# Kernel tuning notes

Measured on AMD Instinct MI355X. Metric: run time of the kernel, lower is better.

## Reference

```python
import jax, jax.numpy as jnp
import numpy as np

B, T, C, HEAD = 4, 4096, 1024, 64
SCALE = 1.0 / (C ** 0.5)  # module divides by embedding_size**0.5, not head_size**0.5


def setup_inputs() -> dict:
    key = jax.random.key(0)
    kx, kq, kk, kv = jax.random.split(key, 4)
    x = jax.random.normal(kx, (B, T, C), dtype=jnp.float32)
    # nn.Linear(C, head_size, bias=False) weights, stored as (C, head_size) for x @ W
    Wq = jax.random.normal(kq, (C, HEAD), dtype=jnp.float32) * (1.0 / np.sqrt(C))
    Wk = jax.random.normal(kk, (C, HEAD), dtype=jnp.float32) * (1.0 / np.sqrt(C))
    Wv = jax.random.normal(kv, (C, HEAD), dtype=jnp.float32) * (1.0 / np.sqrt(C))
    return {"x": x, "Wq": Wq, "Wk": Wk, "Wv": Wv}


def reference(x, Wq, Wk, Wv):
    q = jnp.einsum('btc,ch->bth', x, Wq)  # [B,T,HEAD]
    k = jnp.einsum('btc,ch->bth', x, Wk)
    v = jnp.einsum('btc,ch->bth', x, Wv)
    aff = jnp.einsum('bqh,bkh->bqk', q, k) * SCALE  # [B,T,T]
    causal = jnp.tril(jnp.ones((T, T), dtype=bool))
    aff = jnp.where(causal, aff, -jnp.inf)
    p = jax.nn.softmax(aff, axis=-1)  # dropout p=0.0 -> identity
    return jnp.einsum('bqk,bkh->bqh', p, v)  # [B,T,HEAD]
```

## Files before the change

### kernel.cpp

```cpp
#include <hip/hip_runtime.h>

#define T_SEQ 4096
#define NBATCH 4
#define CDIM 1024
#define NHEAD 64
#define SCALE (1.0f / 32.0f)
#define LOG2E 1.4426950408889634f
#define BT (NBATCH * T_SEQ)
#define NW 8
#define WREG 8960
#define PSTR 9
#define THR2 11.0f

typedef __bf16 bf16x8 __attribute__((ext_vector_type(8)));
typedef float f32x4 __attribute__((ext_vector_type(4)));
typedef unsigned long long u64;

__device__ __forceinline__ unsigned short f2bf(float f) {
  union { float f; unsigned u; } x;
  x.f = f;
  unsigned r = x.u + 0x7FFFu + ((x.u >> 16) & 1u);
  return (unsigned short)(r >> 16);
}

__device__ __forceinline__ unsigned cvt_pk(float lo, float hi) {
  unsigned d;
  asm("v_cvt_pk_bf16_f32 %0, %1, %2" : "=v"(d) : "v"(lo), "v"(hi));
  return d;
}

__device__ __forceinline__ f32x4 mfma16(bf16x8 a, bf16x8 b, f32x4 c) {
  return __builtin_amdgcn_mfma_f32_16x16x32_bf16(a, b, c, 0, 0, 0);
}

__device__ __forceinline__ bf16x8 ones8() {
  bf16x8 v;
  for (int j = 0; j < 8; ++j) v[j] = (__bf16)1.0f;
  return v;
}

__global__ void prep_w(const float* __restrict__ Wq, const float* __restrict__ Wk,
                       const float* __restrict__ Wv, unsigned short* __restrict__ Wt) {
  int c = blockIdx.x;
  const float* W = (c < 64) ? Wq : (c < 128) ? Wk : Wv;
  int cc = c & 63;
  float sc = (c < 64) ? (SCALE * LOG2E) : 1.0f;
  for (int k = threadIdx.x; k < CDIM; k += blockDim.x)
    Wt[c * CDIM + k] = f2bf(W[k * NHEAD + cc] * sc);
}

__global__ __launch_bounds__(256) void proj_qkv(
    const float* __restrict__ x, const unsigned short* __restrict__ Wt,
    unsigned short* __restrict__ qws, unsigned short* __restrict__ kws,
    unsigned short* __restrict__ vtws) {
  __shared__ unsigned short xlds[32][136];
  const int tid = threadIdx.x;
  const int lane = tid & 63;
  const int w = tid >> 6;
  const int g = lane >> 4;
  const int c15 = lane & 15;
  const int rb = blockIdx.x * 32;

  f32x4 acc[2][3];
  for (int i = 0; i < 2; i++)
    for (int j = 0; j < 3; j++) acc[i][j] = (f32x4){0.f, 0.f, 0.f, 0.f};

  const int sr = tid >> 3;
  const int scc = (tid & 7) * 16;
  const float* xrow = x + (size_t)(rb + sr) * CDIM + scc;

  float4 cur[4];
  for (int i = 0; i < 4; i++) cur[i] = *(const float4*)(xrow + i * 4);

  for (int k0 = 0; k0 < CDIM; k0 += 128) {
    unsigned short pk[16];
    for (int i = 0; i < 4; i++) {
      pk[i * 4 + 0] = f2bf(cur[i].x);
      pk[i * 4 + 1] = f2bf(cur[i].y);
      pk[i * 4 + 2] = f2bf(cur[i].z);
      pk[i * 4 + 3] = f2bf(cur[i].w);
    }
    *(bf16x8*)&xlds[sr][scc] = *(bf16x8*)&pk[0];
    *(bf16x8*)&xlds[sr][scc + 8] = *(bf16x8*)&pk[8];
    __syncthreads();
    if (k0 + 128 < CDIM)
      for (int i = 0; i < 4; i++)
        cur[i] = *(const float4*)(xrow + k0 + 128 + i * 4);

    for (int kk = 0; kk < 4; kk++) {
      bf16x8 a[2];
      for (int mt = 0; mt < 2; mt++)
        a[mt] = *(bf16x8*)&xlds[mt * 16 + c15][kk * 32 + g * 8];
      for (int bn = 0; bn < 3; bn++) {
        int col = w * 48 + bn * 16 + c15;
        bf16x8 bfrag =
            *(const bf16x8*)&Wt[(size_t)col * CDIM + k0 + kk * 32 + g * 8];
        for (int mt = 0; mt < 2; mt++)
          acc[mt][bn] = mfma16(a[mt], bfrag, acc[mt][bn]);
      }
    }
    __syncthreads();
  }

  for (int mt = 0; mt < 2; mt++)
    for (int bn = 0; bn < 3; bn++) {
      int col = w * 48 + bn * 16 + c15;
      int row0 = rb + mt * 16 + 4 * g;
      for (int r = 0; r < 4; r++) {
        unsigned short v = f2bf(acc[mt][bn][r]);
        int t = row0 + r;
        if (col < 64)
          qws[(size_t)t * 64 + col] = v;
        else if (col < 128)
          kws[(size_t)t * 64 + (col - 64)] = v;
        else
          vtws[(size_t)(col - 128) * BT + t] = v;
      }
    }
}

__global__ __launch_bounds__(512, 2) void attn_fwd(
    const unsigned short* __restrict__ qws, const unsigned short* __restrict__ kws,
    const unsigned short* __restrict__ vtws, float* __restrict__ out) {
  __shared__ __align__(16) char smem[NW * WREG];
  const int tid = threadIdx.x;
  const int lane = tid & 63;
  const int w = tid >> 6;
  const int g = lane >> 4;
  const int c = lane & 15;
  const int b = blockIdx.x >> 6;
  const int pi = blockIdx.x & 63;
  const size_t rowbase = (size_t)b * T_SEQ;
  char* wbase = smem + w * WREG;
  u64* pl = (u64*)wbase;
  const bf16x8 vone = ones8();

  for (int half = 0; half < 2; ++half) {
    const int qt = half ? (127 - pi) : pi;
    const int qb = qt * 32;
    const int nsteps = qt + 1;

    bf16x8 qf[2][2];
    for (int mi = 0; mi < 2; mi++)
      for (int hc = 0; hc < 2; hc++)
        qf[mi][hc] = *(const bf16x8*)&qws[(rowbase + qb + mi * 16 + c) * 64 +
                                          hc * 32 + g * 8];

    f32x4 o[2][4];
    f32x4 o5[2];
    float mrow[2];
    for (int mi = 0; mi < 2; mi++) {
      for (int nt = 0; nt < 4; nt++) o[mi][nt] = (f32x4){0.f, 0.f, 0.f, 0.f};
      o5[mi] = (f32x4){0.f, 0.f, 0.f, 0.f};
      mrow[mi] = -1e30f;
    }

    auto PREF = [&](int st, bf16x8 (&k0)[2], bf16x8 (&k1)[2], bf16x8 (&v)[4]) {
      const int kt = st * 32;
      for (int kn = 0; kn < 2; kn++) {
        k0[kn] = *(const bf16x8*)&kws[(rowbase + kt + kn * 16 + c) * 64 + g * 8];
        k1[kn] =
            *(const bf16x8*)&kws[(rowbase + kt + kn * 16 + c) * 64 + 32 + g * 8];
      }
      for (int nt = 0; nt < 4; nt++)
        v[nt] = *(const bf16x8*)&vtws[(size_t)(nt * 16 + c) * BT + rowbase + kt +
                                      g * 8];
    };

    auto COMPUTE = [&](int st, bf16x8 (&k0)[2], bf16x8 (&k1)[2], bf16x8 (&v)[4]) {
      const int kt = st * 32;
      f32x4 sv[2][2];
      for (int mi = 0; mi < 2; mi++)
        for (int kn = 0; kn < 2; kn++) {
          f32x4 z = (f32x4){0.f, 0.f, 0.f, 0.f};
          z = mfma16(k0[kn], qf[mi][0], z);
          sv[mi][kn] = mfma16(k1[kn], qf[mi][1], z);
        }

      if (st == nsteps - 1) {
        for (int mi = 0; mi < 2; mi++)
          for (int kn = 0; kn < 2; kn++)
            for (int r = 0; r < 4; r++) {
              int key = kt + kn * 16 + 4 * g + r;
              int qr = qb + mi * 16 + c;
              if (key > qr) sv[mi][kn][r] = -1e30f;
            }
      }

      for (int mi = 0; mi < 2; mi++) {
        float t = fmaxf(
            fmaxf(fmaxf(sv[mi][0][0], sv[mi][0][1]),
                  fmaxf(sv[mi][0][2], sv[mi][0][3])),
            fmaxf(fmaxf(sv[mi][1][0], sv[mi][1][1]),
                  fmaxf(sv[mi][1][2], sv[mi][1][3])));
        t = fmaxf(t, __shfl_xor(t, 16));
        t = fmaxf(t, __shfl_xor(t, 32));
        if (__any(t > mrow[mi] + THR2)) {
          float mn = fmaxf(mrow[mi], t);
          float a = exp2f(mrow[mi] - mn);
          mrow[mi] = mn;
          for (int nt = 0; nt < 4; nt++) o[mi][nt] *= a;
          o5[mi] *= a;
        }
        float p[8];
        for (int kn = 0; kn < 2; kn++)
          for (int r = 0; r < 4; r++)
            p[kn * 4 + r] = exp2f(sv[mi][kn][r] - mrow[mi]);
        unsigned d0 = cvt_pk(p[0], p[1]);
        unsigned d1 = cvt_pk(p[2], p[3]);
        unsigned d2 = cvt_pk(p[4], p[5]);
        unsigned d3 = cvt_pk(p[6], p[7]);
        int row = mi * 16 + c;
        pl[row * PSTR + g] = ((u64)d1 << 32) | d0;
        pl[row * PSTR + 4 + g] = ((u64)d3 << 32) | d2;
      }

      asm volatile("" ::: "memory");

      for (int mi = 0; mi < 2; mi++) {
        union { u64 q[2]; bf16x8 v8; } pu;
        pu.q[0] = pl[(mi * 16 + c) * PSTR + 2 * g];
        pu.q[1] = pl[(mi * 16 + c) * PSTR + 2 * g + 1];
        bf16x8 pa = pu.v8;
        for (int nt = 0; nt < 4; nt++)
          o[mi][nt] = mfma16(v[nt], pa, o[mi][nt]);
        o5[mi] = mfma16(vone, pa, o5[mi]);
      }
    };

    bf16x8 ka0[2], ka1[2], va[4], kb0[2], kb1[2], vb[4];
    if (w < nsteps) PREF(w, ka0, ka1, va);
    int st = w;
    while (st < nsteps) {
      if (st + NW < nsteps) PREF(st + NW, kb0, kb1, vb);
      COMPUTE(st, ka0, ka1, va);
      st += NW;
      if (st >= nsteps) break;
      if (st + NW < nsteps) PREF(st + NW, ka0, ka1, va);
      COMPUTE(st, kb0, kb1, vb);
      st += NW;
    }

    float* ow = (float*)wbase;
    float* mw = (float*)(wbase + 8704);
    float* lw = (float*)(wbase + 8832);
    for (int mi = 0; mi < 2; mi++)
      for (int nt = 0; nt < 4; nt++)
        for (int r = 0; r < 4; r++)
          ow[(mi * 16 + c) * 68 + nt * 16 + 4 * g + r] = o[mi][nt][r];
    if (g == 0)
      for (int mi = 0; mi < 2; mi++) {
        mw[mi * 16 + c] = mrow[mi];
        lw[mi * 16 + c] = o5[mi][0];
      }
    __syncthreads();

    for (int i = 0; i < 4; i++) {
      int e = tid + i * 512;
      int row = e >> 6;
      int d = e & 63;
      float M = -1e30f;
      for (int ww = 0; ww < NW; ww++)
        M = fmaxf(M, ((const float*)(smem + ww * WREG + 8704))[row]);
      float L = 0.f, O = 0.f;
      for (int ww = 0; ww < NW; ww++) {
        float mv = ((const float*)(smem + ww * WREG + 8704))[row];
        float f = exp2f(mv - M);
        L += f * ((const float*)(smem + ww * WREG + 8832))[row];
        O += f * ((const float*)(smem + ww * WREG))[row * 68 + d];
      }
      out[(rowbase + qb + row) * 64 + d] = O / L;
    }
    __syncthreads();
  }
}

extern "C" void kernel_launch(void* const* d_in, const int* in_sizes, int n_in,
                              void* d_out, int out_size, void* d_ws, size_t ws_size,
                              hipStream_t stream) {
  const float* x = (const float*)d_in[0];
  const float* Wq = (const float*)d_in[1];
  const float* Wk = (const float*)d_in[2];
  const float* Wv = (const float*)d_in[3];
  float* out = (float*)d_out;

  char* ws = (char*)d_ws;
  unsigned short* Wt = (unsigned short*)(ws);
  unsigned short* qws = (unsigned short*)(ws + 393216);
  unsigned short* kws = (unsigned short*)(ws + 393216 + 2097152);
  unsigned short* vtws = (unsigned short*)(ws + 393216 + 2 * 2097152);

  prep_w<<<dim3(192), dim3(256), 0, stream>>>(Wq, Wk, Wv, Wt);
  proj_qkv<<<dim3(512), dim3(256), 0, stream>>>(x, Wt, qws, kws, vtws);
  attn_fwd<<<dim3(256), dim3(512), 0, stream>>>(qws, kws, vtws, out);
}
```

Baseline: 85.24 us.

## Process 64-key tiles per wave step and drop explicit K/V prefetch double-buffering

Each wave now handles a 64-key block per iteration instead of 32. That means four score MFMA column tiles and two PV k-slices per step, and the P staging stride is widened to hold 16 u64 per row. The hand-rolled double-buffered PREF/COMPUTE loop is replaced by a simple loop that loads K and V at the top of each step. The aim is to halve the per-step overhead: max reduction, shuffles, rescale checks and loop control. The cost is coarser causal granularity, with up to 32 extra masked keys per tile. Short query tiles also leave more of the 8 waves idle, and load latency is no longer hidden by explicit prefetch.

```diff
diff --git a/kernel.cpp b/kernel.cpp
--- a/kernel.cpp
+++ b/kernel.cpp
@@ -9,7 +9,7 @@
 #define BT (NBATCH * T_SEQ)
 #define NW 8
 #define WREG 8960
-#define PSTR 9
+#define PSTR 17
 #define THR2 11.0f
 
 typedef __bf16 bf16x8 __attribute__((ext_vector_type(8)));
@@ -138,7 +138,7 @@
   for (int half = 0; half < 2; ++half) {
     const int qt = half ? (127 - pi) : pi;
     const int qb = qt * 32;
-    const int nsteps = qt + 1;
+    const int nsteps = (qb >> 6) + 1;
 
     bf16x8 qf[2][2];
     for (int mi = 0; mi < 2; mi++)
@@ -155,31 +155,30 @@
       mrow[mi] = -1e30f;
     }
 
-    auto PREF = [&](int st, bf16x8 (&k0)[2], bf16x8 (&k1)[2], bf16x8 (&v)[4]) {
-      const int kt = st * 32;
-      for (int kn = 0; kn < 2; kn++) {
-        k0[kn] = *(const bf16x8*)&kws[(rowbase + kt + kn * 16 + c) * 64 + g * 8];
-        k1[kn] =
+    for (int st = w; st < nsteps; st += NW) {
+      const int kt = st * 64;
+      bf16x8 kc0[4], kc1[4], vc[2][4];
+      for (int kn = 0; kn < 4; kn++) {
+        kc0[kn] = *(const bf16x8*)&kws[(rowbase + kt + kn * 16 + c) * 64 + g * 8];
+        kc1[kn] =
             *(const bf16x8*)&kws[(rowbase + kt + kn * 16 + c) * 64 + 32 + g * 8];
       }
-      for (int nt = 0; nt < 4; nt++)
-        v[nt] = *(const bf16x8*)&vtws[(size_t)(nt * 16 + c) * BT + rowbase + kt +
-                                      g * 8];
-    };
-
-    auto COMPUTE = [&](int st, bf16x8 (&k0)[2], bf16x8 (&k1)[2], bf16x8 (&v)[4]) {
-      const int kt = st * 32;
-      f32x4 sv[2][2];
+      for (int ks = 0; ks < 2; ks++)
+        for (int nt = 0; nt < 4; nt++)
+          vc[ks][nt] = *(const bf16x8*)&vtws[(size_t)(nt * 16 + c) * BT + rowbase +
+                                             kt + ks * 32 + g * 8];
+
+      f32x4 sv[2][4];
       for (int mi = 0; mi < 2; mi++)
-        for (int kn = 0; kn < 2; kn++) {
+        for (int kn = 0; kn < 4; kn++) {
           f32x4 z = (f32x4){0.f, 0.f, 0.f, 0.f};
-          z = mfma16(k0[kn], qf[mi][0], z);
-          sv[mi][kn] = mfma16(k1[kn], qf[mi][1], z);
+          z = mfma16(kc0[kn], qf[mi][0], z);
+          sv[mi][kn] = mfma16(kc1[kn], qf[mi][1], z);
         }
 
       if (st == nsteps - 1) {
         for (int mi = 0; mi < 2; mi++)
-          for (int kn = 0; kn < 2; kn++)
+          for (int kn = 0; kn < 4; kn++)
             for (int r = 0; r < 4; r++) {
               int key = kt + kn * 16 + 4 * g + r;
               int qr = qb + mi * 16 + c;
@@ -188,11 +187,15 @@
       }
 
       for (int mi = 0; mi < 2; mi++) {
-        float t = fmaxf(
-            fmaxf(fmaxf(sv[mi][0][0], sv[mi][0][1]),
-                  fmaxf(sv[mi][0][2], sv[mi][0][3])),
-            fmaxf(fmaxf(sv[mi][1][0], sv[mi][1][1]),
-                  fmaxf(sv[mi][1][2], sv[mi][1][3])));
+        float t0 = fmaxf(fmaxf(sv[mi][0][0], sv[mi][0][1]),
+                         fmaxf(sv[mi][0][2], sv[mi][0][3]));
+        float t1 = fmaxf(fmaxf(sv[mi][1][0], sv[mi][1][1]),
+                         fmaxf(sv[mi][1][2], sv[mi][1][3]));
+        float t2 = fmaxf(fmaxf(sv[mi][2][0], sv[mi][2][1]),
+                         fmaxf(sv[mi][2][2], sv[mi][2][3]));
+        float t3 = fmaxf(fmaxf(sv[mi][3][0], sv[mi][3][1]),
+                         fmaxf(sv[mi][3][2], sv[mi][3][3]));
+        float t = fmaxf(fmaxf(t0, t1), fmaxf(t2, t3));
         t = fmaxf(t, __shfl_xor(t, 16));
         t = fmaxf(t, __shfl_xor(t, 32));
         if (__any(t > mrow[mi] + THR2)) {
@@ -202,43 +205,32 @@
           for (int nt = 0; nt < 4; nt++) o[mi][nt] *= a;
           o5[mi] *= a;
         }
-        float p[8];
-        for (int kn = 0; kn < 2; kn++)
-          for (int r = 0; r < 4; r++)
-            p[kn * 4 + r] = exp2f(sv[mi][kn][r] - mrow[mi]);
-        unsigned d0 = cvt_pk(p[0], p[1]);
-        unsigned d1 = cvt_pk(p[2], p[3]);
-        unsigned d2 = cvt_pk(p[4], p[5]);
-        unsigned d3 = cvt_pk(p[6], p[7]);
         int row = mi * 16 + c;
-        pl[row * PSTR + g] = ((u64)d1 << 32) | d0;
-        pl[row * PSTR + 4 + g] = ((u64)d3 << 32) | d2;
+        for (int kn = 0; kn < 4; kn++) {
+          float p0 = exp2f(sv[mi][kn][0] - mrow[mi]);
+          float p1 = exp2f(sv[mi][kn][1] - mrow[mi]);
+          float p2 = exp2f(sv[mi][kn][2] - mrow[mi]);
+          float p3 = exp2f(sv[mi][kn][3] - mrow[mi]);
+          unsigned dlo = cvt_pk(p0, p1);
+          unsigned dhi = cvt_pk(p2, p3);
+          pl[row * PSTR + kn * 4 + g] = ((u64)dhi << 32) | dlo;
+        }
       }
 
       asm volatile("" ::: "memory");
 
       for (int mi = 0; mi < 2; mi++) {
-        union { u64 q[2]; bf16x8 v8; } pu;
-        pu.q[0] = pl[(mi * 16 + c) * PSTR + 2 * g];
-        pu.q[1] = pl[(mi * 16 + c) * PSTR + 2 * g + 1];
-        bf16x8 pa = pu.v8;
-        for (int nt = 0; nt < 4; nt++)
-          o[mi][nt] = mfma16(v[nt], pa, o[mi][nt]);
-        o5[mi] = mfma16(vone, pa, o5[mi]);
-      }
-    };
-
-    bf16x8 ka0[2], ka1[2], va[4], kb0[2], kb1[2], vb[4];
-    if (w < nsteps) PREF(w, ka0, ka1, va);
-    int st = w;
-    while (st < nsteps) {
-      if (st + NW < nsteps) PREF(st + NW, kb0, kb1, vb);
-      COMPUTE(st, ka0, ka1, va);
-      st += NW;
-      if (st >= nsteps) break;
-      if (st + NW < nsteps) PREF(st + NW, ka0, ka1, va);
-      COMPUTE(st, kb0, kb1, vb);
-      st += NW;
+        int row = mi * 16 + c;
+        for (int ks = 0; ks < 2; ks++) {
+          union { u64 q[2]; bf16x8 v8; } pu;
+          pu.q[0] = pl[row * PSTR + ks * 8 + 2 * g];
+          pu.q[1] = pl[row * PSTR + ks * 8 + 2 * g + 1];
+          bf16x8 pa = pu.v8;
+          for (int nt = 0; nt < 4; nt++)
+            o[mi][nt] = mfma16(vc[ks][nt], pa, o[mi][nt]);
+          o5[mi] = mfma16(vone, pa, o5[mi]);
+        }
+      }
     }
 
     float* ow = (float*)wbase;
```

Measured after the change: 80.49 us. 1.06x faster.
